# Optimization experiments

Hardware: AMD Instinct MI355X
Metric: run time of the kernel (lower is better)

The kernel has to match this reference:

```python
import jax, jax.numpy as jnp
import numpy as np
from jax.ops import segment_sum

N_NODES = 100000
N_EDGES = 3200000
DIM = 256
N_CLASSES = 32
N_GRAPHS = 64


def setup_inputs() -> dict:
    key = jax.random.key(0)
    k1, k2, k3, k4, k5 = jax.random.split(key, 5)
    x = jax.random.normal(k1, (N_NODES, DIM), dtype=jnp.float32)
    W = jax.random.normal(k2, (DIM, N_CLASSES), dtype=jnp.float32) / np.sqrt(DIM)
    b = jax.random.normal(k3, (N_CLASSES,), dtype=jnp.float32) * 0.01
    edge_index = jax.random.randint(k4, (2, N_EDGES), 0, N_NODES, dtype=jnp.int64)
    batch = jnp.sort(jax.random.randint(k5, (N_NODES,), 0, N_GRAPHS, dtype=jnp.int64))
    return {"x": x, "W": W, "b": b, "edge_index": edge_index, "batch": batch}


def reference(x, W, b, edge_index, batch):
    N = x.shape[0]
    # GCNConv: linear transform (no bias), then normalized aggregation, then bias
    h = x @ W  # [N, C]
    # add self loops (PyG default add_self_loops=True)
    loop = jnp.arange(N, dtype=edge_index.dtype)
    src = jnp.concatenate([edge_index[0], loop])  # source (message sender)
    dst = jnp.concatenate([edge_index[1], loop])  # target (aggregation site)
    # symmetric normalization: deg computed at target with unit edge weights
    deg = segment_sum(jnp.ones_like(dst, dtype=h.dtype), dst, num_segments=N)
    dinv = jnp.where(deg > 0, jax.lax.rsqrt(deg), 0.0)
    norm = dinv[src] * dinv[dst]  # [E+N]
    msg = h[src] * norm[:, None]  # gather + scale
    out = segment_sum(msg, dst, num_segments=N) + b  # scatter-add, bias after agg
    # global_mean_pool: segment mean over graphs
    cnt = segment_sum(jnp.ones((N,), dtype=out.dtype), batch, num_segments=N_GRAPHS)
    sums = segment_sum(out, batch, num_segments=N_GRAPHS)
    return sums / jnp.maximum(cnt, 1.0)[:, None]
```

## Files before the change

### kernel.cpp

```cpp
#include <hip/hip_runtime.h>

#define NN    100000
#define NE    3200000
#define DIMK  256
#define NC    32
#define NG    64

#define ROWS   64
#define NBUCK  1563
#define CAP    2432
#define NB1    512
#define EPB    6250
#define NSL    16
#define MAXG   512

static constexpr size_t OFF_REC    = 0;
static constexpr size_t OFF_DINV   = 15204864;
static constexpr size_t OFF_BTOT   = 15604864;
static constexpr size_t OFF_START  = 15613056;
static constexpr size_t OFF_CTRL   = 15613568;
static constexpr size_t OFF_P2     = 15613696;
static constexpr size_t OFF_PART   = 16662272;
static constexpr size_t OFF_DEGARR = OFF_PART;
static constexpr size_t OFF_CNT    = OFF_PART + 400000;
static constexpr size_t OFF_EXC    = OFF_PART + 3601024;

__device__ __forceinline__ int idx_at(const void* p, long i, bool i64) {
    return i64 ? (int)((const long long*)p)[i] : ((const int*)p)[i];
}

__device__ __forceinline__ bool detect_i64(const void* ei) {
    const int* w = (const int*)ei;
    return (w[1] == 0) & (w[3] == 0) & (w[5] == 0) &
           (w[7] == 0) & (w[9] == 0) & (w[11] == 0);
}

__global__ __launch_bounds__(256) void k_pre(const void* __restrict__ ei,
        unsigned int* __restrict__ parts, int* __restrict__ cnt) {
    __shared__ unsigned int h[12500];
    const bool i64 = detect_i64(ei);
    const int b = blockIdx.x;
    if (b < 256) {
        const int hh = b >> 7;
        const int sl = b & 127;
        const int lo = hh * 50000, hi = lo + 50000;
        for (int t = threadIdx.x; t < 12500; t += 256) h[t] = 0u;
        __syncthreads();
        const int e0 = sl * 25000;
        for (int e = e0 + threadIdx.x; e < e0 + 25000; e += 256) {
            int d = idx_at(ei, (long)NE + e, i64);
            if (d >= lo && d < hi) {
                int r = d - lo;
                atomicAdd(&h[r >> 2], 1u << ((r & 3) * 8));
            }
        }
        __syncthreads();
        for (int t = threadIdx.x; t < 12500; t += 256)
            parts[(size_t)b * 12500 + t] = h[t];
    } else {
        const int k = b - 256;
        for (int t = threadIdx.x; t < NBUCK; t += 256) h[t] = 0u;
        __syncthreads();
        const int e0 = k * EPB;
        for (int e = e0 + threadIdx.x; e < e0 + EPB; e += 256) {
            int s = idx_at(ei, e, i64);
            atomicAdd(&h[s >> 6], 1u);
        }
        __syncthreads();
        for (int t = threadIdx.x; t < NBUCK; t += 256)
            cnt[t * NB1 + k] = (int)h[t];
    }
}

__global__ __launch_bounds__(512) void k_mid(const unsigned int* __restrict__ parts,
        unsigned int* __restrict__ degarr, float* __restrict__ dinv,
        const void* __restrict__ batch, const void* __restrict__ ei,
        int* __restrict__ start, const int* __restrict__ cnt,
        int* __restrict__ exc, int* __restrict__ btot) {
    __shared__ int s[512];
    const int b = blockIdx.x;
    const int t = threadIdx.x;
    if (b < 49) {
        int i = b * 512 + t;
        if (i >= 25000) return;
        int h = (i >= 12500) ? 1 : 0;
        int w = i - h * 12500;
        int c0 = 0, c1 = 0, c2 = 0, c3 = 0;
        const unsigned int* base = parts + (size_t)(h * 128) * 12500 + w;
#pragma unroll 4
        for (int q = 0; q < 128; ++q) {
            unsigned int v = base[(size_t)q * 12500];
            c0 += v & 255u; c1 += (v >> 8) & 255u; c2 += (v >> 16) & 255u; c3 += v >> 24;
        }
        int node = h * 50000 + w * 4;
        degarr[node]     = 1u + c0;  dinv[node]     = 1.0f / sqrtf((float)(1 + c0));
        degarr[node + 1] = 1u + c1;  dinv[node + 1] = 1.0f / sqrtf((float)(1 + c1));
        degarr[node + 2] = 1u + c2;  dinv[node + 2] = 1.0f / sqrtf((float)(1 + c2));
        degarr[node + 3] = 1u + c3;  dinv[node + 3] = 1.0f / sqrtf((float)(1 + c3));
    } else if (b < 245) {
        const bool i64 = detect_i64(ei);
        int i = (b - 49) * 512 + t;
        if (i >= NN) return;
        int bi = idx_at(batch, i, i64);
        int bp = (i == 0) ? -1 : idx_at(batch, i - 1, i64);
        for (int g = bp + 1; g <= bi; ++g) start[g] = i;
        if (i == NN - 1)
            for (int g = bi + 1; g <= NG; ++g) start[g] = NN;
    } else {
        const int bkt = b - 245;
        int v = cnt[bkt * NB1 + t];
        s[t] = v;
        __syncthreads();
        for (int off = 1; off < 512; off <<= 1) {
            int u = (t >= off) ? s[t - off] : 0;
            __syncthreads();
            s[t] += u;
            __syncthreads();
        }
        exc[bkt * NB1 + t] = bkt * CAP + (s[t] - v);
        if (t == 511) btot[bkt] = s[511];
    }
}

__global__ __launch_bounds__(256) void k_place(const void* __restrict__ ei,
        const void* __restrict__ batch, const unsigned int* __restrict__ degarr,
        const int* __restrict__ exc, unsigned int* __restrict__ rec,
        int* __restrict__ ctrl) {
    __shared__ unsigned int lc[NBUCK];
    __shared__ int lbase[NBUCK];
    const bool i64 = detect_i64(ei);
    const int k = blockIdx.x;
    if (k == 0 && threadIdx.x == 0) ctrl[1] = 0;
    for (int t = threadIdx.x; t < NBUCK; t += 256) {
        lc[t] = 0u;
        lbase[t] = exc[t * NB1 + k];
    }
    __syncthreads();
    const int e0 = k * EPB;
    for (int e = e0 + threadIdx.x; e < e0 + EPB; e += 256) {
        int s = idx_at(ei, e, i64);
        int d = idx_at(ei, (long)NE + e, i64);
        int g = idx_at(batch, d, i64);
        unsigned int deg = min(degarr[d], 1048575u);
        int b = s >> 6;
        unsigned int r = atomicAdd(&lc[b], 1u);
        rec[lbase[b] + (int)r] = (deg << 12) | (unsigned)(g * 64 + (s & 63));
    }
}

__global__ __launch_bounds__(512, 2) void k_fused(
        const float* __restrict__ x, const float* __restrict__ dinv,
        const void* __restrict__ batch, const void* __restrict__ ei,
        const unsigned int* __restrict__ rec, const int* __restrict__ btot,
        float* __restrict__ part, int* __restrict__ ctrl) {
    __shared__ __align__(16) float Ach[64 * ROWS];
    __shared__ int sbkt;
    const bool i64 = detect_i64(ei);
    const int tid  = threadIdx.x;
    const int gi   = tid >> 6;
    const int lane = tid & 63;

    float acc[8][4];
#pragma unroll
    for (int g = 0; g < 8; ++g)
#pragma unroll
        for (int d = 0; d < 4; ++d) acc[g][d] = 0.0f;

    const float4* x4 = (const float4*)x;
    float4* Ach4 = (float4*)Ach;
    const float4 z4 = make_float4(0.f, 0.f, 0.f, 0.f);
    const int jmax = NN - 1;

    for (;;) {
        if (tid == 0) sbkt = atomicAdd(&ctrl[1], 1);
        __syncthreads();
        const int bkt = sbkt;
        if (bkt >= NBUCK) break;
        const int j0 = bkt * ROWS;

        Ach4[tid] = z4;
        Ach4[tid + 512] = z4;
        __syncthreads();
        if (tid < ROWS) {
            int j = j0 + tid;
            if (j < NN) Ach[idx_at(batch, j, i64) * 64 + tid] = dinv[j];
        }
        __syncthreads();
        {
            const int rb = bkt * CAP;
            const int re = rb + btot[bkt];
            for (int r = rb + tid; r < re; r += 512) {
                unsigned int q = rec[r];
                float val = 1.0f / sqrtf((float)(q >> 12));
                atomicAdd(&Ach[q & 4095u], val);
            }
        }
        __syncthreads();
        float areg[8];
        {
            float dv = dinv[min(j0 + lane, jmax)];
#pragma unroll
            for (int q = 0; q < 8; ++q)
                areg[q] = Ach[(gi * 8 + q) * 64 + lane] * dv;
        }
        __syncthreads();

        if (bkt < NBUCK - 1) {
            const float4* xp = x4 + (size_t)j0 * 64 + lane;
            float4 buf[8];
#pragma unroll
            for (int k = 0; k < 8; ++k) buf[k] = xp[k * 64];
            xp += 512;
            for (int c = 0; c < 8; ++c) {
#pragma unroll
                for (int jj = 0; jj < 8; ++jj) {
                    float4 xv = buf[jj];
                    buf[jj] = xp[jj * 64];
#pragma unroll
                    for (int q = 0; q < 8; ++q) {
                        float aq = __int_as_float(__builtin_amdgcn_readlane(
                            __float_as_int(areg[q]), c * 8 + jj));
                        acc[q][0] = fmaf(aq, xv.x, acc[q][0]);
                        acc[q][1] = fmaf(aq, xv.y, acc[q][1]);
                        acc[q][2] = fmaf(aq, xv.z, acc[q][2]);
                        acc[q][3] = fmaf(aq, xv.w, acc[q][3]);
                    }
                }
                xp += 512;
            }
        } else {
            float4 xv = x4[(size_t)min(j0, jmax) * 64 + lane];
#pragma unroll 4
            for (int jj = 0; jj < ROWS; ++jj) {
                float4 xn = x4[(size_t)min(j0 + jj + 1, jmax) * 64 + lane];
#pragma unroll
                for (int q = 0; q < 8; ++q) {
                    float aq = __int_as_float(__builtin_amdgcn_readlane(
                        __float_as_int(areg[q]), jj));
                    acc[q][0] = fmaf(aq, xv.x, acc[q][0]);
                    acc[q][1] = fmaf(aq, xv.y, acc[q][1]);
                    acc[q][2] = fmaf(aq, xv.z, acc[q][2]);
                    acc[q][3] = fmaf(aq, xv.w, acc[q][3]);
                }
                xv = xn;
            }
        }
    }

    float* p = part + (size_t)blockIdx.x * (NG * DIMK);
#pragma unroll
    for (int g = 0; g < 8; ++g) {
        float4 w = make_float4(acc[g][0], acc[g][1], acc[g][2], acc[g][3]);
        ((float4*)(p + (gi * 8 + g) * DIMK))[lane] = w;
    }
}

__global__ __launch_bounds__(256) void k_reduce1(const float4* __restrict__ part,
        float4* __restrict__ p2, int nblk) {
    int id = blockIdx.x * 256 + threadIdx.x;
    int c4 = id & 4095;
    int sl = id >> 12;
    int span = (nblk + NSL - 1) / NSL;
    int b0 = sl * span, b1 = min(b0 + span, nblk);
    float4 s = make_float4(0.f, 0.f, 0.f, 0.f);
    for (int b = b0; b < b1; ++b) {
        float4 v = part[(size_t)b * 4096 + c4];
        s.x += v.x; s.y += v.y; s.z += v.z; s.w += v.w;
    }
    p2[(size_t)sl * 4096 + c4] = s;
}

__global__ __launch_bounds__(256) void k_final(const float* __restrict__ p2,
        const float* __restrict__ W, const float* __restrict__ bias,
        const int* __restrict__ start, float* __restrict__ out) {
    __shared__ float Sb[8 * DIMK];
    const int tid = threadIdx.x, b = blockIdx.x;
    for (int t = tid; t < 8 * DIMK; t += 256) {
        int gl = t >> 8, d = t & 255;
        float s = 0.f;
#pragma unroll
        for (int sl = 0; sl < NSL; ++sl)
            s += p2[(size_t)sl * (NG * DIMK) + (b * 8 + gl) * DIMK + d];
        Sb[t] = s;
    }
    __syncthreads();
    int g = tid >> 5, c = tid & 31;
    float sum = 0.f;
#pragma unroll 8
    for (int d = 0; d < DIMK; ++d)
        sum = fmaf(Sb[g * DIMK + d], W[d * NC + c], sum);
    int gg = b * 8 + g;
    float cn = (float)max(start[gg + 1] - start[gg], 1);
    out[gg * NC + c] = sum / cn + bias[c];
}

extern "C" void kernel_launch(void* const* d_in, const int* in_sizes, int n_in,
                              void* d_out, int out_size, void* d_ws, size_t ws_size,
                              hipStream_t stream) {
    const float* x    = (const float*)d_in[0];
    const float* W    = (const float*)d_in[1];
    const float* bias = (const float*)d_in[2];
    const void*  ei   = d_in[3];
    const void*  batch= d_in[4];
    float* out = (float*)d_out;

    char* ws = (char*)d_ws;
    unsigned int* rec  = (unsigned int*)(ws + OFF_REC);
    unsigned int* degp = (unsigned int*)(ws + OFF_REC);
    float* dinv  = (float*)(ws + OFF_DINV);
    int*   btot  = (int*)(ws + OFF_BTOT);
    int*   start = (int*)(ws + OFF_START);
    int*   ctrl  = (int*)(ws + OFF_CTRL);
    float* p2    = (float*)(ws + OFF_P2);
    float* part  = (float*)(ws + OFF_PART);
    unsigned int* degarr = (unsigned int*)(ws + OFF_DEGARR);
    int*   cnt   = (int*)(ws + OFF_CNT);
    int*   exc   = (int*)(ws + OFF_EXC);

    long avail = (long)(ws_size - OFF_PART) / 65536;
    int grid = (int)avail;
    if (grid > MAXG) grid = MAXG;
    if (grid < 64) grid = 64;

    k_pre    <<<768, 256, 0, stream>>>(ei, degp, cnt);
    k_mid    <<<1808, 512, 0, stream>>>(degp, degarr, dinv, batch, ei, start,
                                        cnt, exc, btot);
    k_place  <<<NB1, 256, 0, stream>>>(ei, batch, degarr, exc, rec, ctrl);
    k_fused  <<<grid, 512, 0, stream>>>(x, dinv, batch, ei, rec, btot, part, ctrl);
    k_reduce1<<<256, 256, 0, stream>>>((const float4*)part, (float4*)p2, grid);
    k_final  <<<8, 256, 0, stream>>>(p2, W, bias, start, out);
}
```

Before: 204.3 us.

## Split fused aggregation across four graph-quarter queues with smaller blocks

The fused gather/aggregate kernel now splits the 64 graphs into four quarters. Each block handles one quarter (16 graphs) through its own work-stealing counter, uses 256 threads, and keeps a smaller accumulator, which allows more resident blocks and a larger grid. The reduction and final kernels are reindexed to the per-quarter partial layout. The cost is that each row bucket's x slice is read four times (once per quarter) and each quarter block rescans the full record list, filtering out records for other quarters.

```diff
diff --git a/kernel.cpp b/kernel.cpp
--- a/kernel.cpp
+++ b/kernel.cpp
@@ -11,8 +11,7 @@
 #define CAP    2432
 #define NB1    512
 #define EPB    6250
-#define NSL    16
-#define MAXG   512
+#define MAXG   2048
 
 static constexpr size_t OFF_REC    = 0;
 static constexpr size_t OFF_DINV   = 15204864;
@@ -130,7 +129,7 @@
     __shared__ int lbase[NBUCK];
     const bool i64 = detect_i64(ei);
     const int k = blockIdx.x;
-    if (k == 0 && threadIdx.x == 0) ctrl[1] = 0;
+    if (k == 0 && threadIdx.x < 4) ctrl[1 + threadIdx.x] = 0;
     for (int t = threadIdx.x; t < NBUCK; t += 256) {
         lc[t] = 0u;
         lbase[t] = exc[t * NB1 + k];
@@ -148,21 +147,22 @@
     }
 }
 
-__global__ __launch_bounds__(512, 2) void k_fused(
+__global__ __launch_bounds__(256, 6) void k_fused(
         const float* __restrict__ x, const float* __restrict__ dinv,
         const void* __restrict__ batch, const void* __restrict__ ei,
         const unsigned int* __restrict__ rec, const int* __restrict__ btot,
         float* __restrict__ part, int* __restrict__ ctrl) {
-    __shared__ __align__(16) float Ach[64 * ROWS];
+    __shared__ __align__(16) float Ach[16 * 64];
     __shared__ int sbkt;
     const bool i64 = detect_i64(ei);
     const int tid  = threadIdx.x;
-    const int gi   = tid >> 6;
+    const int wid  = tid >> 6;
     const int lane = tid & 63;
-
-    float acc[8][4];
-#pragma unroll
-    for (int g = 0; g < 8; ++g)
+    const int myq  = blockIdx.x & 3;
+
+    float acc[4][4];
+#pragma unroll
+    for (int g = 0; g < 4; ++g)
 #pragma unroll
         for (int d = 0; d < 4; ++d) acc[g][d] = 0.0f;
 
@@ -172,69 +172,52 @@
     const int jmax = NN - 1;
 
     for (;;) {
-        if (tid == 0) sbkt = atomicAdd(&ctrl[1], 1);
+        if (tid == 0) sbkt = atomicAdd(&ctrl[1 + myq], 1);
         __syncthreads();
         const int bkt = sbkt;
         if (bkt >= NBUCK) break;
         const int j0 = bkt * ROWS;
 
         Ach4[tid] = z4;
-        Ach4[tid + 512] = z4;
         __syncthreads();
         if (tid < ROWS) {
             int j = j0 + tid;
-            if (j < NN) Ach[idx_at(batch, j, i64) * 64 + tid] = dinv[j];
+            if (j < NN) {
+                int g = idx_at(batch, j, i64);
+                if ((g >> 4) == myq)
+                    Ach[(g & 15) * 64 + tid] = dinv[j];
+            }
         }
         __syncthreads();
         {
             const int rb = bkt * CAP;
             const int re = rb + btot[bkt];
-            for (int r = rb + tid; r < re; r += 512) {
+            for (int r = rb + tid; r < re; r += 256) {
                 unsigned int q = rec[r];
-                float val = 1.0f / sqrtf((float)(q >> 12));
-                atomicAdd(&Ach[q & 4095u], val);
-            }
-        }
-        __syncthreads();
-        float areg[8];
+                unsigned int idx = q & 4095u;
+                if ((int)(idx >> 10) == myq) {
+                    float val = 1.0f / sqrtf((float)(q >> 12));
+                    atomicAdd(&Ach[idx & 1023u], val);
+                }
+            }
+        }
+        __syncthreads();
+        float areg[4];
         {
             float dv = dinv[min(j0 + lane, jmax)];
 #pragma unroll
-            for (int q = 0; q < 8; ++q)
-                areg[q] = Ach[(gi * 8 + q) * 64 + lane] * dv;
-        }
-        __syncthreads();
-
-        if (bkt < NBUCK - 1) {
+            for (int q = 0; q < 4; ++q)
+                areg[q] = Ach[(wid * 4 + q) * 64 + lane] * dv;
+        }
+        __syncthreads();
+
+        if (j0 + ROWS <= NN) {
             const float4* xp = x4 + (size_t)j0 * 64 + lane;
-            float4 buf[8];
-#pragma unroll
-            for (int k = 0; k < 8; ++k) buf[k] = xp[k * 64];
-            xp += 512;
-            for (int c = 0; c < 8; ++c) {
-#pragma unroll
-                for (int jj = 0; jj < 8; ++jj) {
-                    float4 xv = buf[jj];
-                    buf[jj] = xp[jj * 64];
-#pragma unroll
-                    for (int q = 0; q < 8; ++q) {
-                        float aq = __int_as_float(__builtin_amdgcn_readlane(
-                            __float_as_int(areg[q]), c * 8 + jj));
-                        acc[q][0] = fmaf(aq, xv.x, acc[q][0]);
-                        acc[q][1] = fmaf(aq, xv.y, acc[q][1]);
-                        acc[q][2] = fmaf(aq, xv.z, acc[q][2]);
-                        acc[q][3] = fmaf(aq, xv.w, acc[q][3]);
-                    }
-                }
-                xp += 512;
-            }
-        } else {
-            float4 xv = x4[(size_t)min(j0, jmax) * 64 + lane];
-#pragma unroll 4
+#pragma unroll 8
             for (int jj = 0; jj < ROWS; ++jj) {
-                float4 xn = x4[(size_t)min(j0 + jj + 1, jmax) * 64 + lane];
-#pragma unroll
-                for (int q = 0; q < 8; ++q) {
+                float4 xv = xp[jj * 64];
+#pragma unroll
+                for (int q = 0; q < 4; ++q) {
                     float aq = __int_as_float(__builtin_amdgcn_readlane(
                         __float_as_int(areg[q]), jj));
                     acc[q][0] = fmaf(aq, xv.x, acc[q][0]);
@@ -242,32 +225,46 @@
                     acc[q][2] = fmaf(aq, xv.z, acc[q][2]);
                     acc[q][3] = fmaf(aq, xv.w, acc[q][3]);
                 }
-                xv = xn;
-            }
-        }
-    }
-
-    float* p = part + (size_t)blockIdx.x * (NG * DIMK);
-#pragma unroll
-    for (int g = 0; g < 8; ++g) {
+            }
+        } else {
+#pragma unroll 4
+            for (int jj = 0; jj < ROWS; ++jj) {
+                float4 xv = x4[(size_t)min(j0 + jj, jmax) * 64 + lane];
+#pragma unroll
+                for (int q = 0; q < 4; ++q) {
+                    float aq = __int_as_float(__builtin_amdgcn_readlane(
+                        __float_as_int(areg[q]), jj));
+                    acc[q][0] = fmaf(aq, xv.x, acc[q][0]);
+                    acc[q][1] = fmaf(aq, xv.y, acc[q][1]);
+                    acc[q][2] = fmaf(aq, xv.z, acc[q][2]);
+                    acc[q][3] = fmaf(aq, xv.w, acc[q][3]);
+                }
+            }
+        }
+    }
+
+    float* p = part + (size_t)blockIdx.x * (16 * DIMK);
+#pragma unroll
+    for (int g = 0; g < 4; ++g) {
         float4 w = make_float4(acc[g][0], acc[g][1], acc[g][2], acc[g][3]);
-        ((float4*)(p + (gi * 8 + g) * DIMK))[lane] = w;
+        ((float4*)(p + (wid * 4 + g) * DIMK))[lane] = w;
     }
 }
 
 __global__ __launch_bounds__(256) void k_reduce1(const float4* __restrict__ part,
-        float4* __restrict__ p2, int nblk) {
+        float4* __restrict__ p2, int grid) {
     int id = blockIdx.x * 256 + threadIdx.x;
-    int c4 = id & 4095;
-    int sl = id >> 12;
-    int span = (nblk + NSL - 1) / NSL;
-    int b0 = sl * span, b1 = min(b0 + span, nblk);
+    int c4 = id & 1023;
+    int sl = (id >> 10) & 15;
+    int q  = id >> 14;
+    int nq = (grid - q + 3) >> 2;
+    int k0 = sl * nq / 16, k1 = (sl + 1) * nq / 16;
     float4 s = make_float4(0.f, 0.f, 0.f, 0.f);
-    for (int b = b0; b < b1; ++b) {
-        float4 v = part[(size_t)b * 4096 + c4];
+    for (int k = k0; k < k1; ++k) {
+        float4 v = part[(size_t)(q + 4 * k) * 1024 + c4];
         s.x += v.x; s.y += v.y; s.z += v.z; s.w += v.w;
     }
-    p2[(size_t)sl * 4096 + c4] = s;
+    p2[(size_t)(q * 16 + sl) * 1024 + c4] = s;
 }
 
 __global__ __launch_bounds__(256) void k_final(const float* __restrict__ p2,
@@ -277,10 +274,12 @@
     const int tid = threadIdx.x, b = blockIdx.x;
     for (int t = tid; t < 8 * DIMK; t += 256) {
         int gl = t >> 8, d = t & 255;
+        int g = b * 8 + gl;
+        int q = g >> 4, g16 = g & 15;
         float s = 0.f;
 #pragma unroll
-        for (int sl = 0; sl < NSL; ++sl)
-            s += p2[(size_t)sl * (NG * DIMK) + (b * 8 + gl) * DIMK + d];
+        for (int sl = 0; sl < 16; ++sl)
+            s += p2[(size_t)(q * 16 + sl) * 4096 + g16 * 256 + d];
         Sb[t] = s;
     }
     __syncthreads();
@@ -317,7 +316,7 @@
     int*   cnt   = (int*)(ws + OFF_CNT);
     int*   exc   = (int*)(ws + OFF_EXC);
 
-    long avail = (long)(ws_size - OFF_PART) / 65536;
+    long avail = (long)(ws_size - OFF_PART) / 16384;
     int grid = (int)avail;
     if (grid > MAXG) grid = MAXG;
     if (grid < 64) grid = 64;
@@ -326,7 +325,7 @@
     k_mid    <<<1808, 512, 0, stream>>>(degp, degarr, dinv, batch, ei, start,
                                         cnt, exc, btot);
     k_place  <<<NB1, 256, 0, stream>>>(ei, batch, degarr, exc, rec, ctrl);
-    k_fused  <<<grid, 512, 0, stream>>>(x, dinv, batch, ei, rec, btot, part, ctrl);
+    k_fused  <<<grid, 256, 0, stream>>>(x, dinv, batch, ei, rec, btot, part, ctrl);
     k_reduce1<<<256, 256, 0, stream>>>((const float4*)part, (float4*)p2, grid);
     k_final  <<<8, 256, 0, stream>>>(p2, W, bias, start, out);
 }
```

New measurement: 280.6 us. 37.4% more time.

## Double k_fused block to 1024 threads splitting bucket rows across two halves

Applied to the files above, without the earlier changes.

Launches k_fused with 1024 threads per block. Each half of the block handles 32 of the 64 rows in a bucket, and the two halves' accumulators are combined through shared memory before the partial sums are written. The explicit register prefetch pipeline for x is replaced by a simple unrolled loop. The goal is more in-flight loads per bucket and higher occupancy for the memory-bound GEMV-like pass. The cost is extra syncs in the epilogue and possible register pressure under launch_bounds(1024,2).

```diff
diff --git a/kernel.cpp b/kernel.cpp
--- a/kernel.cpp
+++ b/kernel.cpp
@@ -148,7 +148,7 @@
     }
 }
 
-__global__ __launch_bounds__(512, 2) void k_fused(
+__global__ __launch_bounds__(1024, 2) void k_fused(
         const float* __restrict__ x, const float* __restrict__ dinv,
         const void* __restrict__ batch, const void* __restrict__ ei,
         const unsigned int* __restrict__ rec, const int* __restrict__ btot,
@@ -157,8 +157,10 @@
     __shared__ int sbkt;
     const bool i64 = detect_i64(ei);
     const int tid  = threadIdx.x;
-    const int gi   = tid >> 6;
+    const int rh   = tid >> 9;
+    const int gi   = (tid >> 6) & 7;
     const int lane = tid & 63;
+    const int rbase = rh << 5;
 
     float acc[8][4];
 #pragma unroll
@@ -179,7 +181,6 @@
         const int j0 = bkt * ROWS;
 
         Ach4[tid] = z4;
-        Ach4[tid + 512] = z4;
         __syncthreads();
         if (tid < ROWS) {
             int j = j0 + tid;
@@ -189,7 +190,7 @@
         {
             const int rb = bkt * CAP;
             const int re = rb + btot[bkt];
-            for (int r = rb + tid; r < re; r += 512) {
+            for (int r = rb + tid; r < re; r += 1024) {
                 unsigned int q = rec[r];
                 float val = 1.0f / sqrtf((float)(q >> 12));
                 atomicAdd(&Ach[q & 4095u], val);
@@ -205,53 +206,61 @@
         }
         __syncthreads();
 
-        if (bkt < NBUCK - 1) {
-            const float4* xp = x4 + (size_t)j0 * 64 + lane;
-            float4 buf[8];
-#pragma unroll
-            for (int k = 0; k < 8; ++k) buf[k] = xp[k * 64];
-            xp += 512;
-            for (int c = 0; c < 8; ++c) {
-#pragma unroll
-                for (int jj = 0; jj < 8; ++jj) {
-                    float4 xv = buf[jj];
-                    buf[jj] = xp[jj * 64];
-#pragma unroll
-                    for (int q = 0; q < 8; ++q) {
-                        float aq = __int_as_float(__builtin_amdgcn_readlane(
-                            __float_as_int(areg[q]), c * 8 + jj));
-                        acc[q][0] = fmaf(aq, xv.x, acc[q][0]);
-                        acc[q][1] = fmaf(aq, xv.y, acc[q][1]);
-                        acc[q][2] = fmaf(aq, xv.z, acc[q][2]);
-                        acc[q][3] = fmaf(aq, xv.w, acc[q][3]);
-                    }
-                }
-                xp += 512;
-            }
-        } else {
-            float4 xv = x4[(size_t)min(j0, jmax) * 64 + lane];
+        if (j0 + ROWS <= NN) {
+            const float4* xp = x4 + (size_t)(j0 + rbase) * 64 + lane;
 #pragma unroll 4
-            for (int jj = 0; jj < ROWS; ++jj) {
-                float4 xn = x4[(size_t)min(j0 + jj + 1, jmax) * 64 + lane];
+            for (int jj = 0; jj < 32; ++jj) {
+                float4 xv = xp[jj * 64];
 #pragma unroll
                 for (int q = 0; q < 8; ++q) {
                     float aq = __int_as_float(__builtin_amdgcn_readlane(
-                        __float_as_int(areg[q]), jj));
+                        __float_as_int(areg[q]), rbase + jj));
                     acc[q][0] = fmaf(aq, xv.x, acc[q][0]);
                     acc[q][1] = fmaf(aq, xv.y, acc[q][1]);
                     acc[q][2] = fmaf(aq, xv.z, acc[q][2]);
                     acc[q][3] = fmaf(aq, xv.w, acc[q][3]);
                 }
-                xv = xn;
             }
-        }
-    }
-
-    float* p = part + (size_t)blockIdx.x * (NG * DIMK);
+        } else {
+#pragma unroll 4
+            for (int jj = 0; jj < 32; ++jj) {
+                float4 xv = x4[(size_t)min(j0 + rbase + jj, jmax) * 64 + lane];
+#pragma unroll
+                for (int q = 0; q < 8; ++q) {
+                    float aq = __int_as_float(__builtin_amdgcn_readlane(
+                        __float_as_int(areg[q]), rbase + jj));
+                    acc[q][0] = fmaf(aq, xv.x, acc[q][0]);
+                    acc[q][1] = fmaf(aq, xv.y, acc[q][1]);
+                    acc[q][2] = fmaf(aq, xv.z, acc[q][2]);
+                    acc[q][3] = fmaf(aq, xv.w, acc[q][3]);
+                }
+            }
+        }
+    }
+
+    __syncthreads();
 #pragma unroll
     for (int g = 0; g < 8; ++g) {
-        float4 w = make_float4(acc[g][0], acc[g][1], acc[g][2], acc[g][3]);
-        ((float4*)(p + (gi * 8 + g) * DIMK))[lane] = w;
+        if (rh == 1) {
+            Ach4[gi * 64 + lane] = make_float4(acc[g][0], acc[g][1],
+                                               acc[g][2], acc[g][3]);
+        }
+        __syncthreads();
+        if (rh == 0) {
+            float4 v = Ach4[gi * 64 + lane];
+            acc[g][0] += v.x; acc[g][1] += v.y;
+            acc[g][2] += v.z; acc[g][3] += v.w;
+        }
+        __syncthreads();
+    }
+
+    if (rh == 0) {
+        float* p = part + (size_t)blockIdx.x * (NG * DIMK);
+#pragma unroll
+        for (int g = 0; g < 8; ++g) {
+            float4 w = make_float4(acc[g][0], acc[g][1], acc[g][2], acc[g][3]);
+            ((float4*)(p + (gi * 8 + g) * DIMK))[lane] = w;
+        }
     }
 }
 
@@ -326,7 +335,7 @@
     k_mid    <<<1808, 512, 0, stream>>>(degp, degarr, dinv, batch, ei, start,
                                         cnt, exc, btot);
     k_place  <<<NB1, 256, 0, stream>>>(ei, batch, degarr, exc, rec, ctrl);
-    k_fused  <<<grid, 512, 0, stream>>>(x, dinv, batch, ei, rec, btot, part, ctrl);
+    k_fused  <<<grid, 1024, 0, stream>>>(x, dinv, batch, ei, rec, btot, part, ctrl);
     k_reduce1<<<256, 256, 0, stream>>>((const float4*)part, (float4*)p2, grid);
     k_final  <<<8, 256, 0, stream>>>(p2, W, bias, start, out);
 }
```

After: 222.6 us. 1.09x slower.
